# Performance work log

Hardware: AMD Instinct MI355X
Metric: run time of the kernel (lower is better)

## Reference

```python
import jax, jax.numpy as jnp
import numpy as np

B, S, H = 1, 4096, 2048
NH, HD = 16, 128  # num_heads, head_dim = H // NH


def setup_inputs() -> dict:
    key = jax.random.key(0)
    k1, k2, k3 = jax.random.split(key, 3)
    x = jax.random.normal(k1, (B, S, H), dtype=jnp.float32)
    w_qkv = jax.random.normal(k2, (3 * H, H), dtype=jnp.float32) * (1.0 / np.sqrt(H))
    w_out = jax.random.normal(k3, (H, H), dtype=jnp.float32) * (1.0 / np.sqrt(H))
    return {"x": x, "w_qkv": w_qkv, "w_out": w_out}


def reference(x, w_qkv, w_out):
    b, s, _ = x.shape
    # qkv projection: torch Linear computes x @ W^T
    qkv = jnp.einsum('bsh,oh->bso', x, w_qkv)
    qkv = qkv.reshape(b, s, 3, NH, HD).transpose(2, 0, 3, 1, 4)  # [3,B,NH,S,HD]
    q, k, v = qkv[0], qkv[1], qkv[2]
    # world_size == 1 -> single ring step == full attention with online softmax
    scores = jnp.einsum('bhqd,bhkd->bhqk', q, k) / np.sqrt(HD)
    m = jnp.max(scores, axis=-1, keepdims=True)          # running max (single step)
    p = jnp.exp(scores - m)                              # scores_exp
    out = jnp.einsum('bhqk,bhkd->bhqd', p, v)
    denom = jnp.sum(p, axis=-1, keepdims=True) + 1e-8    # running_sum + eps
    out = out / denom
    out = out.transpose(0, 2, 1, 3).reshape(b, s, H)     # [B,S,H]
    return jnp.einsum('bsh,oh->bso', out, w_out)
```

## Files before the change

### kernel.cpp

```cpp
#include <hip/hip_runtime.h>
#include <stdint.h>

typedef __attribute__((ext_vector_type(4))) float f32x4;
typedef __attribute__((ext_vector_type(16))) float f32x16;
typedef __attribute__((ext_vector_type(8))) short bf16x8;
typedef unsigned short u16;

#define MFMA(a, b, c) __builtin_amdgcn_mfma_f32_16x16x32_bf16(a, b, c, 0, 0, 0)
#define MFMA32(a, b, c) __builtin_amdgcn_mfma_f32_32x32x16_bf16(a, b, c, 0, 0, 0)
#define EXP2(x) __builtin_amdgcn_exp2f(x)

__device__ __forceinline__ u16 f2bf(float f) {
  union { float f; unsigned u; } x; x.f = f;
  unsigned r = x.u + 0x7fffu + ((x.u >> 16) & 1u);
  return (u16)(r >> 16);
}

__device__ __forceinline__ unsigned cvtpk(float lo, float hi) {
  unsigned r;
  asm("v_cvt_pk_bf16_f32 %0, %1, %2" : "=v"(r) : "v"(lo), "v"(hi));
  return r;
}

__device__ __forceinline__ void pl32swap(unsigned& a, unsigned& b) {
  asm volatile("v_permlane32_swap_b32 %0, %1" : "+v"(a), "+v"(b));
}

__device__ __forceinline__ void gload16(const void* g, void* l) {
  __builtin_amdgcn_global_load_lds(
      (const __attribute__((address_space(1))) unsigned int*)g,
      (__attribute__((address_space(3))) unsigned int*)l, 16, 0, 0);
}

__global__ void __launch_bounds__(256) cast_bf16(const float* __restrict__ in,
                                                 u16* __restrict__ out, int n4) {
  int i = blockIdx.x * 256 + threadIdx.x;
  if (i >= n4) return;
  float4 v = reinterpret_cast<const float4*>(in)[i];
  ushort4 o;
  o.x = f2bf(v.x); o.y = f2bf(v.y); o.z = f2bf(v.z); o.w = f2bf(v.w);
  reinterpret_cast<ushort4*>(out)[i] = o;
}

template <int EPI>
__global__ void __launch_bounds__(256, 2)
gemm_bt(const u16* __restrict__ A, const u16* __restrict__ B,
        void* __restrict__ C0, void* __restrict__ C1, void* __restrict__ C2,
        int M, int N, int K, int MB) {
  __shared__ alignas(16) u16 sm[8192];
  const int tid = threadIdx.x;
  const int w = tid >> 6, lane = tid & 63;
  const int lr = lane & 15, g = lane >> 4;
  const int mb = blockIdx.x % MB, nb = blockIdx.x / MB;
  const int m0 = mb * 128, n0 = nb * 128;

  const u16* src[4];
  u16* dst[4];
#pragma unroll
  for (int i = 0; i < 4; ++i) {
    int c = w * 4 + i;
    int r = (c & 7) * 16 + (lane >> 2);
    int sb = (lane & 3) ^ ((r >> 1) & 3);
    src[i] = (c < 8) ? (A + (size_t)(m0 + r) * K + sb * 8)
                     : (B + (size_t)(n0 + r) * K + sb * 8);
    dst[i] = &sm[c * 512];
  }

  f32x4 acc[4][4];
#pragma unroll
  for (int x = 0; x < 4; ++x)
#pragma unroll
    for (int y = 0; y < 4; ++y) acc[x][y] = f32x4{0.f, 0.f, 0.f, 0.f};

  const int rowb = (w >> 1) * 64, colb = (w & 1) * 64;
  const int nk = K >> 5;
  for (int kt = 0; kt < nk; ++kt) {
#pragma unroll
    for (int i = 0; i < 4; ++i) gload16(src[i] + kt * 32, dst[i]);
    __syncthreads();
    bf16x8 af[4], bfr[4];
#pragma unroll
    for (int mi = 0; mi < 4; ++mi) {
      int r = rowb + mi * 16 + lr;
      af[mi] = *(const bf16x8*)((const char*)sm + r * 64 +
                                ((g * 16) ^ (((r >> 1) & 3) << 4)));
    }
#pragma unroll
    for (int ni = 0; ni < 4; ++ni) {
      int r = colb + ni * 16 + lr;
      bfr[ni] = *(const bf16x8*)((const char*)sm + 8192 + r * 64 +
                                 ((g * 16) ^ (((r >> 1) & 3) << 4)));
    }
#pragma unroll
    for (int mi = 0; mi < 4; ++mi)
#pragma unroll
      for (int ni = 0; ni < 4; ++ni)
        acc[mi][ni] = MFMA(af[mi], bfr[ni], acc[mi][ni]);
    __syncthreads();
  }

  if (EPI == 0) {
    u16* qo = (u16*)C0;
    u16* ko = (u16*)C1;
    u16* vo = (u16*)C2;
#pragma unroll
    for (int mi = 0; mi < 4; ++mi) {
      int s0 = m0 + rowb + mi * 16 + g * 4;
#pragma unroll
      for (int ni = 0; ni < 4; ++ni) {
        int n = n0 + colb + ni * 16 + lr;
        int t = n >> 11, hh = (n >> 7) & 15, d = n & 127;
        if (t == 2) {
          ushort4 pk;
          pk.x = f2bf(acc[mi][ni][0]);
          pk.y = f2bf(acc[mi][ni][1]);
          pk.z = f2bf(acc[mi][ni][2]);
          pk.w = f2bf(acc[mi][ni][3]);
          *(ushort4*)(vo + (size_t)(hh * 128 + d) * 4096 + s0) = pk;
        } else {
          u16* dq = (t == 0 ? qo : ko) + (size_t)(hh * 4096 + s0) * 128 + d;
#pragma unroll
          for (int j = 0; j < 4; ++j) dq[(size_t)j * 128] = f2bf(acc[mi][ni][j]);
        }
      }
    }
  } else {
    float* C = (float*)C0;
#pragma unroll
    for (int mi = 0; mi < 4; ++mi)
#pragma unroll
      for (int ni = 0; ni < 4; ++ni) {
        size_t r0 = (size_t)(m0 + rowb + mi * 16 + g * 4);
        int cn = n0 + colb + ni * 16 + lr;
#pragma unroll
        for (int j = 0; j < 4; ++j) C[(r0 + j) * N + cn] = acc[mi][ni][j];
      }
  }
}

__global__ void __launch_bounds__(256, 2)
attn_kernel(const u16* __restrict__ qg, const u16* __restrict__ kg,
            const u16* __restrict__ vtg, u16* __restrict__ og) {
  __shared__ alignas(16) u16 sm[32768];
  const int tid = threadIdx.x;
  const int w = tid >> 6, lane = tid & 63;
  const int ql = lane & 31, hl = lane >> 5;
  const int h = blockIdx.x >> 5;
  const int qb = blockIdx.x & 31;

  const u16* ssrc[8];
  u16* sdst[8];
  size_t sstep;
  if (w < 2) {
    sstep = 64 * 128;
#pragma unroll
    for (int i = 0; i < 8; ++i) {
      int c = (w & 1) * 8 + i;
      int r = c * 4 + (lane >> 4);
      int sb = (lane & 15) ^ (r & 7);
      ssrc[i] = kg + (size_t)(h * 4096 + r) * 128 + sb * 8;
      sdst[i] = &sm[c * 512];
    }
  } else {
    sstep = 64;
#pragma unroll
    for (int i = 0; i < 8; ++i) {
      int c = (w & 1) * 8 + i;
      int r = c * 8 + (lane >> 3);
      int sb = (lane & 7) ^ (r & 7);
      ssrc[i] = vtg + (size_t)(h * 128 + r) * 4096 + sb * 8;
      sdst[i] = &sm[16384 + c * 512];
    }
  }

  const u16* qrow = qg + (size_t)(h * 4096 + qb * 128 + w * 32 + ql) * 128 + hl * 8;
  bf16x8 qf[8];
#pragma unroll
  for (int s = 0; s < 8; ++s) qf[s] = *(const bf16x8*)(qrow + s * 16);

  f32x16 of[4];
#pragma unroll
  for (int i = 0; i < 4; ++i)
#pragma unroll
    for (int r = 0; r < 16; ++r) of[i][r] = 0.f;
  float mrun = -1e30f, lsum = 0.f;
  const float sc2 = 0.08838834764831845f * 1.4426950408889634f;

#pragma unroll
  for (int i = 0; i < 8; ++i) gload16(ssrc[i], sdst[i]);

  for (int t = 0; t < 64; ++t) {
    const int cur = t & 1;
    asm volatile("s_waitcnt vmcnt(0)" ::: "memory");
    __builtin_amdgcn_s_barrier();
    asm volatile("" ::: "memory");
    if (t + 1 < 64) {
      const int nb = (t + 1) & 1;
#pragma unroll
      for (int i = 0; i < 8; ++i)
        gload16(ssrc[i] + (size_t)(t + 1) * sstep, sdst[i] + nb * 8192);
    }
    const char* kbuf = (const char*)sm + cur * 16384;
    const char* vbuf = (const char*)sm + 32768 + cur * 16384;

    f32x16 st0, st1;
#pragma unroll
    for (int r = 0; r < 16; ++r) { st0[r] = 0.f; st1[r] = 0.f; }
    const int swz = (ql & 7) << 4;
#pragma unroll
    for (int s = 0; s < 8; ++s) {
      int off = (s * 32 + hl * 16) ^ swz;
      bf16x8 k0 = *(const bf16x8*)(kbuf + ql * 256 + off);
      bf16x8 k1 = *(const bf16x8*)(kbuf + (32 + ql) * 256 + off);
      st0 = MFMA32(k0, qf[s], st0);
      st1 = MFMA32(k1, qf[s], st1);
    }

    float tmax = -1e30f;
#pragma unroll
    for (int r = 0; r < 16; ++r) tmax = fmaxf(tmax, fmaxf(st0[r], st1[r]));
    tmax = fmaxf(tmax, __shfl_xor(tmax, 32));
    float mnew = fmaxf(mrun, tmax);
    float esc = EXP2((mrun - mnew) * sc2);
    float mb = mnew * sc2;
    float psum = 0.f;
    unsigned pk0[8], pk1[8];
#pragma unroll
    for (int i = 0; i < 8; ++i) {
      float a0 = EXP2(st0[2 * i] * sc2 - mb);
      float b0 = EXP2(st0[2 * i + 1] * sc2 - mb);
      float a1 = EXP2(st1[2 * i] * sc2 - mb);
      float b1 = EXP2(st1[2 * i + 1] * sc2 - mb);
      psum += (a0 + b0) + (a1 + b1);
      pk0[i] = cvtpk(a0, b0);
      pk1[i] = cvtpk(a1, b1);
    }
    psum += __shfl_xor(psum, 32);
    lsum = lsum * esc + psum;
    mrun = mnew;

    pl32swap(pk0[0], pk0[2]); pl32swap(pk0[1], pk0[3]);
    pl32swap(pk0[4], pk0[6]); pl32swap(pk0[5], pk0[7]);
    pl32swap(pk1[0], pk1[2]); pl32swap(pk1[1], pk1[3]);
    pl32swap(pk1[4], pk1[6]); pl32swap(pk1[5], pk1[7]);
    union U { unsigned u[4]; bf16x8 v; };
    U paf[4];
#pragma unroll
    for (int i = 0; i < 4; ++i) { paf[0].u[i] = pk0[i]; paf[1].u[i] = pk0[4 + i]; }
#pragma unroll
    for (int i = 0; i < 4; ++i) { paf[2].u[i] = pk1[i]; paf[3].u[i] = pk1[4 + i]; }

#pragma unroll
    for (int db = 0; db < 4; ++db)
#pragma unroll
      for (int r = 0; r < 16; ++r) of[db][r] *= esc;

#pragma unroll
    for (int db = 0; db < 4; ++db) {
      int rr = db * 32 + ql;
      int vswz = (rr & 7) << 4;
#pragma unroll
      for (int kp = 0; kp < 4; ++kp) {
        bf16x8 vf = *(const bf16x8*)(vbuf + rr * 128 + ((kp * 32 + hl * 16) ^ vswz));
        of[db] = MFMA32(vf, paf[kp].v, of[db]);
      }
    }
    asm volatile("" ::: "memory");
  }

  float linv = 1.f / (lsum + 1e-8f);
  size_t qrow_o = (size_t)(qb * 128 + w * 32 + ql) * 2048 + h * 128;
#pragma unroll
  for (int db = 0; db < 4; ++db)
#pragma unroll
    for (int u = 0; u < 4; ++u) {
      ushort4 pk;
      pk.x = f2bf(of[db][4 * u + 0] * linv);
      pk.y = f2bf(of[db][4 * u + 1] * linv);
      pk.z = f2bf(of[db][4 * u + 2] * linv);
      pk.w = f2bf(of[db][4 * u + 3] * linv);
      *(ushort4*)(og + qrow_o + db * 32 + 8 * u + hl * 4) = pk;
    }
}

extern "C" void kernel_launch(void* const* d_in, const int* in_sizes, int n_in,
                              void* d_out, int out_size, void* d_ws, size_t ws_size,
                              hipStream_t stream) {
  const float* x = (const float*)d_in[0];
  const float* w_qkv = (const float*)d_in[1];
  const float* w_out = (const float*)d_in[2];

  char* ws = (char*)d_ws;
  u16* xb = (u16*)(ws + 0);
  u16* wqkvb = (u16*)(ws + 16777216);
  u16* woutb = (u16*)(ws + 41943040);
  u16* qb = (u16*)(ws + 50331648);
  u16* kb = (u16*)(ws + 67108864);
  u16* vtb = (u16*)(ws + 83886080);
  u16* aob = (u16*)(ws + 100663296);

  cast_bf16<<<8192, 256, 0, stream>>>(x, xb, 2097152);
  cast_bf16<<<12288, 256, 0, stream>>>(w_qkv, wqkvb, 3145728);
  cast_bf16<<<4096, 256, 0, stream>>>(w_out, woutb, 1048576);

  gemm_bt<0><<<32 * 48, 256, 0, stream>>>(xb, wqkvb, qb, kb, vtb, 4096, 6144, 2048, 32);
  attn_kernel<<<512, 256, 0, stream>>>(qb, kb, vtb, aob);
  gemm_bt<1><<<32 * 16, 256, 0, stream>>>(aob, woutb, d_out, nullptr, nullptr, 4096, 2048, 2048, 32);
}
```

Before: 362.0 us.

## Process two query chunks per wave in attention with lazy max rescaling

Each wave now handles 64 query rows (two 32-row chunks) instead of 32, so every K/V tile loaded into shared memory is reused across twice as many queries, halving the block count to 256. The online-softmax rescale is skipped when the new tile max stays within a threshold of the running max, avoiding the accumulator multiply in most iterations. Blocks are remapped with a swizzle across heads, and launch bounds drop to one block per SIMD to allow more registers. The risk is higher register pressure and fewer blocks than CUs (256 blocks), which may underfill the GPU.

```diff
diff --git a/kernel.cpp b/kernel.cpp
--- a/kernel.cpp
+++ b/kernel.cpp
@@ -138,15 +138,16 @@
   }
 }
 
-__global__ void __launch_bounds__(256, 2)
+__global__ void __launch_bounds__(256, 1)
 attn_kernel(const u16* __restrict__ qg, const u16* __restrict__ kg,
             const u16* __restrict__ vtg, u16* __restrict__ og) {
   __shared__ alignas(16) u16 sm[32768];
   const int tid = threadIdx.x;
   const int w = tid >> 6, lane = tid & 63;
   const int ql = lane & 31, hl = lane >> 5;
-  const int h = blockIdx.x >> 5;
-  const int qb = blockIdx.x & 31;
+  const int bsw = (blockIdx.x & 7) * 32 + (blockIdx.x >> 3);
+  const int h = bsw >> 4;
+  const int qb = bsw & 15;
 
   const u16* ssrc[8];
   u16* sdst[8];
@@ -173,18 +174,25 @@
     }
   }
 
-  const u16* qrow = qg + (size_t)(h * 4096 + qb * 128 + w * 32 + ql) * 128 + hl * 8;
-  bf16x8 qf[8];
-#pragma unroll
-  for (int s = 0; s < 8; ++s) qf[s] = *(const bf16x8*)(qrow + s * 16);
-
-  f32x16 of[4];
-#pragma unroll
-  for (int i = 0; i < 4; ++i)
-#pragma unroll
-    for (int r = 0; r < 16; ++r) of[i][r] = 0.f;
-  float mrun = -1e30f, lsum = 0.f;
+  bf16x8 qf[2][4 * 2];
+#pragma unroll
+  for (int qc = 0; qc < 2; ++qc) {
+    const u16* qrow =
+        qg + (size_t)(h * 4096 + qb * 256 + w * 64 + qc * 32 + ql) * 128 + hl * 8;
+#pragma unroll
+    for (int s = 0; s < 8; ++s) qf[qc][s] = *(const bf16x8*)(qrow + s * 16);
+  }
+
+  f32x16 of[2][4];
+#pragma unroll
+  for (int qc = 0; qc < 2; ++qc)
+#pragma unroll
+    for (int i = 0; i < 4; ++i)
+#pragma unroll
+      for (int r = 0; r < 16; ++r) of[qc][i][r] = 0.f;
+  float mrun[2] = {-1e30f, -1e30f}, lsum[2] = {0.f, 0.f};
   const float sc2 = 0.08838834764831845f * 1.4426950408889634f;
+  const float thr = 6.0f / sc2;
 
 #pragma unroll
   for (int i = 0; i < 8; ++i) gload16(ssrc[i], sdst[i]);
@@ -203,57 +211,76 @@
     const char* kbuf = (const char*)sm + cur * 16384;
     const char* vbuf = (const char*)sm + 32768 + cur * 16384;
 
-    f32x16 st0, st1;
-#pragma unroll
-    for (int r = 0; r < 16; ++r) { st0[r] = 0.f; st1[r] = 0.f; }
+    f32x16 st[2][2];
+#pragma unroll
+    for (int qc = 0; qc < 2; ++qc)
+#pragma unroll
+      for (int kb = 0; kb < 2; ++kb)
+#pragma unroll
+        for (int r = 0; r < 16; ++r) st[qc][kb][r] = 0.f;
     const int swz = (ql & 7) << 4;
 #pragma unroll
     for (int s = 0; s < 8; ++s) {
       int off = (s * 32 + hl * 16) ^ swz;
       bf16x8 k0 = *(const bf16x8*)(kbuf + ql * 256 + off);
       bf16x8 k1 = *(const bf16x8*)(kbuf + (32 + ql) * 256 + off);
-      st0 = MFMA32(k0, qf[s], st0);
-      st1 = MFMA32(k1, qf[s], st1);
-    }
-
-    float tmax = -1e30f;
-#pragma unroll
-    for (int r = 0; r < 16; ++r) tmax = fmaxf(tmax, fmaxf(st0[r], st1[r]));
-    tmax = fmaxf(tmax, __shfl_xor(tmax, 32));
-    float mnew = fmaxf(mrun, tmax);
-    float esc = EXP2((mrun - mnew) * sc2);
-    float mb = mnew * sc2;
-    float psum = 0.f;
-    unsigned pk0[8], pk1[8];
-#pragma unroll
-    for (int i = 0; i < 8; ++i) {
-      float a0 = EXP2(st0[2 * i] * sc2 - mb);
-      float b0 = EXP2(st0[2 * i + 1] * sc2 - mb);
-      float a1 = EXP2(st1[2 * i] * sc2 - mb);
-      float b1 = EXP2(st1[2 * i + 1] * sc2 - mb);
-      psum += (a0 + b0) + (a1 + b1);
-      pk0[i] = cvtpk(a0, b0);
-      pk1[i] = cvtpk(a1, b1);
-    }
-    psum += __shfl_xor(psum, 32);
-    lsum = lsum * esc + psum;
-    mrun = mnew;
-
-    pl32swap(pk0[0], pk0[2]); pl32swap(pk0[1], pk0[3]);
-    pl32swap(pk0[4], pk0[6]); pl32swap(pk0[5], pk0[7]);
-    pl32swap(pk1[0], pk1[2]); pl32swap(pk1[1], pk1[3]);
-    pl32swap(pk1[4], pk1[6]); pl32swap(pk1[5], pk1[7]);
+      st[0][0] = MFMA32(k0, qf[0][s], st[0][0]);
+      st[0][1] = MFMA32(k1, qf[0][s], st[0][1]);
+      st[1][0] = MFMA32(k0, qf[1][s], st[1][0]);
+      st[1][1] = MFMA32(k1, qf[1][s], st[1][1]);
+    }
+
     union U { unsigned u[4]; bf16x8 v; };
-    U paf[4];
-#pragma unroll
-    for (int i = 0; i < 4; ++i) { paf[0].u[i] = pk0[i]; paf[1].u[i] = pk0[4 + i]; }
-#pragma unroll
-    for (int i = 0; i < 4; ++i) { paf[2].u[i] = pk1[i]; paf[3].u[i] = pk1[4 + i]; }
-
-#pragma unroll
-    for (int db = 0; db < 4; ++db)
-#pragma unroll
-      for (int r = 0; r < 16; ++r) of[db][r] *= esc;
+    U paf[2][4];
+    float esc[2];
+#pragma unroll
+    for (int qc = 0; qc < 2; ++qc) {
+      float tmax = -1e30f;
+#pragma unroll
+      for (int r = 0; r < 16; ++r)
+        tmax = fmaxf(tmax, fmaxf(st[qc][0][r], st[qc][1][r]));
+      tmax = fmaxf(tmax, __shfl_xor(tmax, 32));
+      float mnew;
+      if (__all(tmax - mrun[qc] <= thr)) {
+        mnew = mrun[qc];
+        esc[qc] = 1.f;
+      } else {
+        mnew = fmaxf(mrun[qc], tmax);
+        esc[qc] = EXP2((mrun[qc] - mnew) * sc2);
+#pragma unroll
+        for (int db = 0; db < 4; ++db)
+#pragma unroll
+          for (int r = 0; r < 16; ++r) of[qc][db][r] *= esc[qc];
+        mrun[qc] = mnew;
+      }
+      float mb = mnew * sc2;
+      float psum = 0.f;
+      unsigned pk0[8], pk1[8];
+#pragma unroll
+      for (int i = 0; i < 8; ++i) {
+        float a0 = EXP2(st[qc][0][2 * i] * sc2 - mb);
+        float b0 = EXP2(st[qc][0][2 * i + 1] * sc2 - mb);
+        float a1 = EXP2(st[qc][1][2 * i] * sc2 - mb);
+        float b1 = EXP2(st[qc][1][2 * i + 1] * sc2 - mb);
+        psum += (a0 + b0) + (a1 + b1);
+        pk0[i] = cvtpk(a0, b0);
+        pk1[i] = cvtpk(a1, b1);
+      }
+      psum += __shfl_xor(psum, 32);
+      lsum[qc] = lsum[qc] * esc[qc] + psum;
+
+      pl32swap(pk0[0], pk0[2]); pl32swap(pk0[1], pk0[3]);
+      pl32swap(pk0[4], pk0[6]); pl32swap(pk0[5], pk0[7]);
+      pl32swap(pk1[0], pk1[2]); pl32swap(pk1[1], pk1[3]);
+      pl32swap(pk1[4], pk1[6]); pl32swap(pk1[5], pk1[7]);
+#pragma unroll
+      for (int i = 0; i < 4; ++i) {
+        paf[qc][0].u[i] = pk0[i];
+        paf[qc][1].u[i] = pk0[4 + i];
+        paf[qc][2].u[i] = pk1[i];
+        paf[qc][3].u[i] = pk1[4 + i];
+      }
+    }
 
 #pragma unroll
     for (int db = 0; db < 4; ++db) {
@@ -262,25 +289,30 @@
 #pragma unroll
       for (int kp = 0; kp < 4; ++kp) {
         bf16x8 vf = *(const bf16x8*)(vbuf + rr * 128 + ((kp * 32 + hl * 16) ^ vswz));
-        of[db] = MFMA32(vf, paf[kp].v, of[db]);
+        of[0][db] = MFMA32(vf, paf[0][kp].v, of[0][db]);
+        of[1][db] = MFMA32(vf, paf[1][kp].v, of[1][db]);
       }
     }
     asm volatile("" ::: "memory");
   }
 
-  float linv = 1.f / (lsum + 1e-8f);
-  size_t qrow_o = (size_t)(qb * 128 + w * 32 + ql) * 2048 + h * 128;
-#pragma unroll
-  for (int db = 0; db < 4; ++db)
-#pragma unroll
-    for (int u = 0; u < 4; ++u) {
-      ushort4 pk;
-      pk.x = f2bf(of[db][4 * u + 0] * linv);
-      pk.y = f2bf(of[db][4 * u + 1] * linv);
-      pk.z = f2bf(of[db][4 * u + 2] * linv);
-      pk.w = f2bf(of[db][4 * u + 3] * linv);
-      *(ushort4*)(og + qrow_o + db * 32 + 8 * u + hl * 4) = pk;
-    }
+#pragma unroll
+  for (int qc = 0; qc < 2; ++qc) {
+    float linv = 1.f / (lsum[qc] + 1e-8f);
+    size_t qrow_o =
+        (size_t)(qb * 256 + w * 64 + qc * 32 + ql) * 2048 + h * 128;
+#pragma unroll
+    for (int db = 0; db < 4; ++db)
+#pragma unroll
+      for (int u = 0; u < 4; ++u) {
+        ushort4 pk;
+        pk.x = f2bf(of[qc][db][4 * u + 0] * linv);
+        pk.y = f2bf(of[qc][db][4 * u + 1] * linv);
+        pk.z = f2bf(of[qc][db][4 * u + 2] * linv);
+        pk.w = f2bf(of[qc][db][4 * u + 3] * linv);
+        *(ushort4*)(og + qrow_o + db * 32 + 8 * u + hl * 4) = pk;
+      }
+  }
 }
 
 extern "C" void kernel_launch(void* const* d_in, const int* in_sizes, int n_in,
@@ -304,6 +336,6 @@
   cast_bf16<<<4096, 256, 0, stream>>>(w_out, woutb, 1048576);
 
   gemm_bt<0><<<32 * 48, 256, 0, stream>>>(xb, wqkvb, qb, kb, vtb, 4096, 6144, 2048, 32);
-  attn_kernel<<<512, 256, 0, stream>>>(qb, kb, vtb, aob);
+  attn_kernel<<<256, 256, 0, stream>>>(qb, kb, vtb, aob);
   gemm_bt<1><<<32 * 16, 256, 0, stream>>>(aob, woutb, d_out, nullptr, nullptr, 4096, 2048, 2048, 32);
 }
```

New measurement: 360.9 us. About the same (-0.3%).
